# Kernel tuning notes

Measured on AMD Instinct MI355X. Metric: run time of the kernel, lower is better.

The kernel has to match this reference:

```python
import jax, jax.numpy as jnp
import numpy as np

B, H = 1024, 256
HP = H // 2  # hyperparams_dim
W_SCALE = 0.08  # kaiming-uniform-like magnitude to keep tanh unsaturated


def setup_inputs() -> dict:
    key = jax.random.key(0)
    ks = jax.random.split(key, 8)
    return {
        "h_0": jax.random.normal(ks[0], (B, 1, H), dtype=jnp.float32),
        "h_t": jax.random.normal(ks[1], (B, 1, H), dtype=jnp.float32),
        "msg": jax.random.normal(ks[2], (B, 1, H), dtype=jnp.float32),
        "c": jax.random.uniform(ks[3], (1,), dtype=jnp.float32),
        "fc1_w": jax.random.normal(ks[4], (HP, H), dtype=jnp.float32) * W_SCALE,
        "fc2_w": jax.random.normal(ks[5], (HP, HP), dtype=jnp.float32) * W_SCALE,
        "fc3_w": jax.random.normal(ks[6], (HP, HP), dtype=jnp.float32) * W_SCALE,
        "fc4_w": jax.random.normal(ks[7], (2 * H * H, HP), dtype=jnp.float32) * W_SCALE,
    }


def reference(h_0, h_t, msg, c, fc1_w, fc2_w, fc3_w, fc4_w):
    # torch code clamps self.c into [0, 1] before use
    cc = jnp.clip(c, 0.0, 1.0)
    h = cc * h_0 + (1.0 - cc) * h_t                     # [B, 1, H]
    x = jnp.tanh(jnp.einsum('bsh,ph->bsp', h, fc1_w))    # [B, 1, HP]
    x = jnp.tanh(jnp.einsum('bsp,qp->bsq', x, fc2_w))    # [B, 1, HP]
    x = jnp.tanh(jnp.einsum('bsq,rq->bsr', x, fc3_w))    # [B, 1, HP]
    f4 = jnp.einsum('bsr,wr->bsw', x, fc4_w)             # [B, 1, 2*H*H]
    g1 = f4[..., : H * H].reshape(-1, H, H)              # [B, H, H]
    g2 = f4[..., H * H :].reshape(-1, H, H)              # [B, H, H]
    # F.linear(msg[i], g) == msg[i] @ g.T, batched over B
    g1_out = jnp.tanh(jnp.einsum('bsh,bkh->bsk', msg, g1))  # [B, 1, H]
    out = jnp.einsum('bsk,bok->bso', g1_out, g2)             # [B, 1, H]
    return out
```

## Files before the change

### kernel.cpp

```cpp
#include <hip/hip_runtime.h>
#include <hip/hip_bf16.h>

#define HDIM 256
#define HPDIM 128

typedef short bf8 __attribute__((ext_vector_type(8)));
typedef float f32x4 __attribute__((ext_vector_type(4)));

__device__ inline unsigned pkbf2(float a, float b) {
  float2 f; f.x = a; f.y = b;
  __hip_bfloat162 h = __float22bfloat162_rn(f);
  unsigned u; __builtin_memcpy(&u, &h, 4); return u;
}
__device__ inline unsigned short bfbits(float v) {
  __hip_bfloat16 h = __float2bfloat16(v);
  unsigned short u; __builtin_memcpy(&u, &h, 2); return u;
}
__device__ inline uint4 pack8u(float4 a, float4 b) {
  uint4 r;
  r.x = pkbf2(a.x, a.y); r.y = pkbf2(a.z, a.w);
  r.z = pkbf2(b.x, b.y); r.w = pkbf2(b.z, b.w);
  return r;
}
__device__ inline float fast_tanh(float x) {
  float t = __expf(2.0f * x);
  return 1.0f - 2.0f * __builtin_amdgcn_rcpf(t + 1.0f);
}
__device__ inline bf8 wfrag(const float* __restrict__ s) {
  float4 a = *(const float4*)s, b = *(const float4*)(s + 4);
  uint4 u = pack8u(a, b);
  bf8 r; __builtin_memcpy(&r, &u, 16); return r;
}

typedef const __attribute__((address_space(1))) unsigned int* gas_ptr;
typedef __attribute__((address_space(3))) unsigned int* las_ptr;
__device__ inline void gld_lds16(const void* g, void* l) {
  __builtin_amdgcn_global_load_lds((gas_ptr)g, (las_ptr)l, 16, 0, 0);
}

__global__ __launch_bounds__(256) void k_prep(
    const float* __restrict__ h0, const float* __restrict__ htv,
    const float* __restrict__ cp,
    const float* __restrict__ w1, const float* __restrict__ w2,
    const float* __restrict__ w3, const float* __restrict__ msg,
    short* __restrict__ x3f, float* __restrict__ msgTT) {
  const int t = threadIdx.x;
  const int bx = blockIdx.x;

  if (bx >= 64) {
    const int b0 = (bx - 64) * 64;
    #pragma unroll
    for (int it = 0; it < 16; ++it) {
      int u = it * 256 + t;
      int bl = u & 63, g = u >> 6;
      float4 v = *(const float4*)(msg + (size_t)(b0 + bl) * HDIM + g * 4);
      *(float4*)(msgTT + (size_t)g * 4096 + (b0 + bl) * 4) = v;
    }
    return;
  }

  __shared__ char hbuf[8192];
  __shared__ char xa[4096];
  __shared__ char xb[4096];
  const int wave = t >> 6, lane = t & 63;
  const int r16 = lane & 15, quad = lane >> 4;
  const int b0 = bx * 16;
  const float cc = fminf(fmaxf(cp[0], 0.f), 1.f);

  #pragma unroll
  for (int it = 0; it < 2; ++it) {
    int flat = it * 2048 + t * 8;
    int row = flat >> 8, col = flat & 255, kb = col >> 3;
    int gi = (b0 + row) * HDIM + col;
    float4 a = *(const float4*)(h0 + gi);
    float4 b = *(const float4*)(htv + gi);
    float4 va, vb;
    va.x = cc*a.x + (1.f-cc)*b.x; va.y = cc*a.y + (1.f-cc)*b.y;
    va.z = cc*a.z + (1.f-cc)*b.z; va.w = cc*a.w + (1.f-cc)*b.w;
    a = *(const float4*)(h0 + gi + 4); b = *(const float4*)(htv + gi + 4);
    vb.x = cc*a.x + (1.f-cc)*b.x; vb.y = cc*a.y + (1.f-cc)*b.y;
    vb.z = cc*a.z + (1.f-cc)*b.z; vb.w = cc*a.w + (1.f-cc)*b.w;
    *(uint4*)(hbuf + row*512 + ((kb ^ (row & 7)) << 4)) = pack8u(va, vb);
  }
  __syncthreads();

  {
    f32x4 acc[2] = {};
    #pragma unroll
    for (int ks = 0; ks < 8; ++ks) {
      bf8 af = *(bf8*)(hbuf + r16*512 + (((ks*4 + quad) ^ (r16 & 7)) << 4));
      #pragma unroll
      for (int nt = 0; nt < 2; ++nt) {
        bf8 bw_ = wfrag(w1 + ((wave*2 + nt)*16 + r16) * 256 + ks*32 + quad*8);
        acc[nt] = __builtin_amdgcn_mfma_f32_16x16x32_bf16(af, bw_, acc[nt], 0, 0, 0);
      }
    }
    #pragma unroll
    for (int nt = 0; nt < 2; ++nt)
      #pragma unroll
      for (int i = 0; i < 4; ++i) {
        int row = quad*4 + i, col = wave*32 + nt*16 + r16;
        *(unsigned short*)(xa + row*256 + (((col >> 3) ^ (row & 7)) << 4) + ((col & 7) << 1))
            = bfbits(fast_tanh(acc[nt][i]));
      }
  }
  __syncthreads();
  {
    f32x4 acc[2] = {};
    #pragma unroll
    for (int ks = 0; ks < 4; ++ks) {
      bf8 af = *(bf8*)(xa + r16*256 + (((ks*4 + quad) ^ (r16 & 7)) << 4));
      #pragma unroll
      for (int nt = 0; nt < 2; ++nt) {
        bf8 bw_ = wfrag(w2 + ((wave*2 + nt)*16 + r16) * 128 + ks*32 + quad*8);
        acc[nt] = __builtin_amdgcn_mfma_f32_16x16x32_bf16(af, bw_, acc[nt], 0, 0, 0);
      }
    }
    #pragma unroll
    for (int nt = 0; nt < 2; ++nt)
      #pragma unroll
      for (int i = 0; i < 4; ++i) {
        int row = quad*4 + i, col = wave*32 + nt*16 + r16;
        *(unsigned short*)(xb + row*256 + (((col >> 3) ^ (row & 7)) << 4) + ((col & 7) << 1))
            = bfbits(fast_tanh(acc[nt][i]));
      }
  }
  __syncthreads();
  {
    f32x4 acc[2] = {};
    #pragma unroll
    for (int ks = 0; ks < 4; ++ks) {
      bf8 af = *(bf8*)(xb + r16*256 + (((ks*4 + quad) ^ (r16 & 7)) << 4));
      #pragma unroll
      for (int nt = 0; nt < 2; ++nt) {
        bf8 bw_ = wfrag(w3 + ((wave*2 + nt)*16 + r16) * 128 + ks*32 + quad*8);
        acc[nt] = __builtin_amdgcn_mfma_f32_16x16x32_bf16(af, bw_, acc[nt], 0, 0, 0);
      }
    }
    #pragma unroll
    for (int nt = 0; nt < 2; ++nt)
      #pragma unroll
      for (int i = 0; i < 4; ++i) {
        int row = quad*4 + i, col = wave*32 + nt*16 + r16;
        *(unsigned short*)(xa + row*256 + (((col >> 3) ^ (row & 7)) << 4) + ((col & 7) << 1))
            = bfbits(fast_tanh(acc[nt][i]));
      }
  }
  __syncthreads();
  {
    int ks = t >> 6, l = t & 63, q2 = l >> 4, rr = l & 15;
    uint4 d = *(uint4*)(xa + rr*256 + (((ks*4 + q2) ^ (rr & 7)) << 4));
    *(uint4*)(x3f + (size_t)((bx*4 + ks)*64 + l)*8) = d;
  }
}

template<int PHASE>
__global__ __launch_bounds__(512, 2) void k_hyper(
    const short* __restrict__ x3f, const float* __restrict__ wTT,
    const float* __restrict__ fc4, float* __restrict__ outp) {
  __shared__ char lds[65536 + 16384];
  char* slab = lds;
  char* ring = lds + 65536;
  const int bxs = blockIdx.x;
  const int h = bxs >> 8;
  const int p = bxs & 255;
  const int kcol = ((p & 7) << 5) | (p >> 3);
  const int t = threadIdx.x, wave = t >> 6, lane = t & 63;
  const int r16 = lane & 15, quad = lane >> 4;
  const int bw = h * 512 + wave * 64;

  const float* src = fc4 + ((size_t)(PHASE ? 65536 : 0) + (size_t)kcol * 256) * HPDIM;

  gld_lds16(src + t * 4, ring + t * 16);

  bf8 xf[4][4];
  #pragma unroll
  for (int nt = 0; nt < 4; ++nt)
    #pragma unroll
    for (int ks = 0; ks < 4; ++ks)
      xf[nt][ks] = *(const bf8*)(x3f +
          (size_t)(((h*32 + wave*4 + nt)*4 + ks)*64 + lane)*8);
  #pragma unroll
  for (int nt = 0; nt < 4; ++nt)
    #pragma unroll
    for (int ks = 0; ks < 4; ++ks)
      asm volatile("" : "+v"(xf[nt][ks]));

  asm volatile("s_waitcnt vmcnt(0) lgkmcnt(0)" ::: "memory");
  __builtin_amdgcn_sched_barrier(0);
  {
    f32x4 v = *(const f32x4*)(ring + t * 16);
    int row = t >> 5, kb = (t & 31) >> 1;
    uint2 o; o.x = pkbf2(v[0], v[1]); o.y = pkbf2(v[2], v[3]);
    *(uint2*)(slab + row * 256 + ((kb ^ (row & 7)) << 4) + (t & 1) * 8) = o;
  }
  gld_lds16(src + 2048 + t * 4, ring + 8192 + t * 16);
  asm volatile("s_waitcnt lgkmcnt(0)" ::: "memory");
  __builtin_amdgcn_sched_barrier(0);
  __builtin_amdgcn_s_barrier();

  float gacc[4] = {0.f, 0.f, 0.f, 0.f};
  const float* wbase = wTT + (size_t)quad * 4096 + (bw + r16) * 4;

  #pragma unroll 1
  for (int c = 0; c < 16; ++c) {
    {
      float4 wv[4];
      #pragma unroll
      for (int nt = 0; nt < 4; ++nt)
        wv[nt] = *(const float4*)(wbase + (size_t)c*16384 + nt*64);
      const int row = c*16 + r16;
      bf8 af[4];
      #pragma unroll
      for (int ks = 0; ks < 4; ++ks)
        af[ks] = *(bf8*)(slab + row*256 + (((ks*4 + quad) ^ (r16 & 7)) << 4));
      #pragma unroll
      for (int nt = 0; nt < 4; ++nt) {
        f32x4 acc = {};
        #pragma unroll
        for (int ks = 0; ks < 4; ++ks)
          acc = __builtin_amdgcn_mfma_f32_16x16x32_bf16(af[ks], xf[nt][ks], acc, 0, 0, 0);
        gacc[nt] += acc[0]*wv[nt].x + acc[1]*wv[nt].y + acc[2]*wv[nt].z + acc[3]*wv[nt].w;
      }
    }
    if (c < 15) {
      asm volatile("s_waitcnt vmcnt(0)" ::: "memory");
      __builtin_amdgcn_sched_barrier(0);
      if (c + 2 < 16)
        gld_lds16(src + (c + 2) * 2048 + t * 4, ring + ((c + 2) & 1) * 8192 + t * 16);
      {
        f32x4 v = *(const f32x4*)(ring + ((c + 1) & 1) * 8192 + t * 16);
        int row = (c + 1) * 16 + (t >> 5), kb = (t & 31) >> 1;
        uint2 o; o.x = pkbf2(v[0], v[1]); o.y = pkbf2(v[2], v[3]);
        *(uint2*)(slab + row * 256 + ((kb ^ ((t >> 5) & 7)) << 4) + (t & 1) * 8) = o;
      }
      asm volatile("s_waitcnt lgkmcnt(0)" ::: "memory");
      __builtin_amdgcn_sched_barrier(0);
      __builtin_amdgcn_s_barrier();
    }
  }

  #pragma unroll
  for (int nt = 0; nt < 4; ++nt) {
    float v = gacc[nt];
    v += __shfl_xor(v, 16);
    v += __shfl_xor(v, 32);
    if (quad == 0) {
      int b = bw + nt*16 + r16;
      if (PHASE == 0) outp[(size_t)(kcol >> 2)*4096 + b*4 + (kcol & 3)] = fast_tanh(v);
      else            outp[b*HDIM + kcol] = v;
    }
  }
}

extern "C" void kernel_launch(void* const* d_in, const int* in_sizes, int n_in,
                              void* d_out, int out_size, void* d_ws, size_t ws_size,
                              hipStream_t stream) {
  const float* h0  = (const float*)d_in[0];
  const float* htt = (const float*)d_in[1];
  const float* msg = (const float*)d_in[2];
  const float* c   = (const float*)d_in[3];
  const float* w1  = (const float*)d_in[4];
  const float* w2  = (const float*)d_in[5];
  const float* w3  = (const float*)d_in[6];
  const float* w4  = (const float*)d_in[7];
  float* out = (float*)d_out;

  short* x3f  = (short*)d_ws;
  float* g1TT = (float*)((char*)d_ws + 262144);
  float* msgTT= (float*)((char*)d_ws + 262144 + 1048576);

  k_prep<<<dim3(80), dim3(256), 0, stream>>>(h0, htt, c, w1, w2, w3, msg,
                                             x3f, msgTT);
  k_hyper<0><<<dim3(512), dim3(512), 0, stream>>>(x3f, msgTT, w4, g1TT);
  k_hyper<1><<<dim3(512), dim3(512), 0, stream>>>(x3f, g1TT, w4, out);
}
```

Baseline: 159.4 us.

## Process both batch halves per block, reusing converted fc4 slab; interleave MFMA chains

Each block now covers all 1024 batch rows instead of one half, so every fc4 column slab is loaded from HBM and converted to bf16 only once instead of twice. The grid shrinks from 512 to 256 blocks. A second pass reuses the resident LDS slab with freshly loaded x fragments for the second batch half. The MFMA loop is also rewritten into four independent accumulator chains wrapped in raised wave priority, which should improve MFMA issue overlap. The cost is fewer blocks (one per CU on 256 CUs) and a serialized second pass per block.

```diff
diff --git a/kernel.cpp b/kernel.cpp
--- a/kernel.cpp
+++ b/kernel.cpp
@@ -161,13 +161,10 @@
   __shared__ char lds[65536 + 16384];
   char* slab = lds;
   char* ring = lds + 65536;
-  const int bxs = blockIdx.x;
-  const int h = bxs >> 8;
-  const int p = bxs & 255;
+  const int p = blockIdx.x;
   const int kcol = ((p & 7) << 5) | (p >> 3);
   const int t = threadIdx.x, wave = t >> 6, lane = t & 63;
   const int r16 = lane & 15, quad = lane >> 4;
-  const int bw = h * 512 + wave * 64;
 
   const float* src = fc4 + ((size_t)(PHASE ? 65536 : 0) + (size_t)kcol * 256) * HPDIM;
 
@@ -179,7 +176,7 @@
     #pragma unroll
     for (int ks = 0; ks < 4; ++ks)
       xf[nt][ks] = *(const bf8*)(x3f +
-          (size_t)(((h*32 + wave*4 + nt)*4 + ks)*64 + lane)*8);
+          (size_t)(((wave*4 + nt)*4 + ks)*64 + lane)*8);
   #pragma unroll
   for (int nt = 0; nt < 4; ++nt)
     #pragma unroll
@@ -200,7 +197,7 @@
   __builtin_amdgcn_s_barrier();
 
   float gacc[4] = {0.f, 0.f, 0.f, 0.f};
-  const float* wbase = wTT + (size_t)quad * 4096 + (bw + r16) * 4;
+  const float* wbase = wTT + (size_t)quad * 4096 + (wave * 64 + r16) * 4;
 
   #pragma unroll 1
   for (int c = 0; c < 16; ++c) {
@@ -214,14 +211,20 @@
       #pragma unroll
       for (int ks = 0; ks < 4; ++ks)
         af[ks] = *(bf8*)(slab + row*256 + (((ks*4 + quad) ^ (r16 & 7)) << 4));
-      #pragma unroll
-      for (int nt = 0; nt < 4; ++nt) {
-        f32x4 acc = {};
-        #pragma unroll
-        for (int ks = 0; ks < 4; ++ks)
-          acc = __builtin_amdgcn_mfma_f32_16x16x32_bf16(af[ks], xf[nt][ks], acc, 0, 0, 0);
-        gacc[nt] += acc[0]*wv[nt].x + acc[1]*wv[nt].y + acc[2]*wv[nt].z + acc[3]*wv[nt].w;
-      }
+      __builtin_amdgcn_s_setprio(1);
+      f32x4 acc0 = {}, acc1 = {}, acc2 = {}, acc3 = {};
+      #pragma unroll
+      for (int ks = 0; ks < 4; ++ks) {
+        acc0 = __builtin_amdgcn_mfma_f32_16x16x32_bf16(af[ks], xf[0][ks], acc0, 0, 0, 0);
+        acc1 = __builtin_amdgcn_mfma_f32_16x16x32_bf16(af[ks], xf[1][ks], acc1, 0, 0, 0);
+        acc2 = __builtin_amdgcn_mfma_f32_16x16x32_bf16(af[ks], xf[2][ks], acc2, 0, 0, 0);
+        acc3 = __builtin_amdgcn_mfma_f32_16x16x32_bf16(af[ks], xf[3][ks], acc3, 0, 0, 0);
+      }
+      __builtin_amdgcn_s_setprio(0);
+      gacc[0] += acc0[0]*wv[0].x + acc0[1]*wv[0].y + acc0[2]*wv[0].z + acc0[3]*wv[0].w;
+      gacc[1] += acc1[0]*wv[1].x + acc1[1]*wv[1].y + acc1[2]*wv[1].z + acc1[3]*wv[1].w;
+      gacc[2] += acc2[0]*wv[2].x + acc2[1]*wv[2].y + acc2[2]*wv[2].z + acc2[3]*wv[2].w;
+      gacc[3] += acc3[0]*wv[3].x + acc3[1]*wv[3].y + acc3[2]*wv[3].z + acc3[3]*wv[3].w;
     }
     if (c < 15) {
       asm volatile("s_waitcnt vmcnt(0)" ::: "memory");
@@ -239,14 +242,65 @@
       __builtin_amdgcn_s_barrier();
     }
   }
-
   #pragma unroll
   for (int nt = 0; nt < 4; ++nt) {
     float v = gacc[nt];
     v += __shfl_xor(v, 16);
     v += __shfl_xor(v, 32);
     if (quad == 0) {
-      int b = bw + nt*16 + r16;
+      int b = wave*64 + nt*16 + r16;
+      if (PHASE == 0) outp[(size_t)(kcol >> 2)*4096 + b*4 + (kcol & 3)] = fast_tanh(v);
+      else            outp[b*HDIM + kcol] = v;
+    }
+  }
+
+  #pragma unroll
+  for (int nt = 0; nt < 4; ++nt)
+    #pragma unroll
+    for (int ks = 0; ks < 4; ++ks)
+      xf[nt][ks] = *(const bf8*)(x3f +
+          (size_t)(((32 + wave*4 + nt)*4 + ks)*64 + lane)*8);
+  #pragma unroll
+  for (int nt = 0; nt < 4; ++nt)
+    #pragma unroll
+    for (int ks = 0; ks < 4; ++ks)
+      asm volatile("" : "+v"(xf[nt][ks]));
+  gacc[0] = gacc[1] = gacc[2] = gacc[3] = 0.f;
+  const float* wbase2 = wTT + (size_t)quad * 4096 + (512 + wave * 64 + r16) * 4;
+
+  #pragma unroll 1
+  for (int hg = 0; hg < 16; ++hg) {
+    float4 wv[4];
+    #pragma unroll
+    for (int nt = 0; nt < 4; ++nt)
+      wv[nt] = *(const float4*)(wbase2 + (size_t)hg*16384 + nt*64);
+    const int row = hg*16 + r16;
+    bf8 af[4];
+    #pragma unroll
+    for (int ks = 0; ks < 4; ++ks)
+      af[ks] = *(bf8*)(slab + row*256 + (((ks*4 + quad) ^ (r16 & 7)) << 4));
+    __builtin_amdgcn_s_setprio(1);
+    f32x4 acc0 = {}, acc1 = {}, acc2 = {}, acc3 = {};
+    #pragma unroll
+    for (int ks = 0; ks < 4; ++ks) {
+      acc0 = __builtin_amdgcn_mfma_f32_16x16x32_bf16(af[ks], xf[0][ks], acc0, 0, 0, 0);
+      acc1 = __builtin_amdgcn_mfma_f32_16x16x32_bf16(af[ks], xf[1][ks], acc1, 0, 0, 0);
+      acc2 = __builtin_amdgcn_mfma_f32_16x16x32_bf16(af[ks], xf[2][ks], acc2, 0, 0, 0);
+      acc3 = __builtin_amdgcn_mfma_f32_16x16x32_bf16(af[ks], xf[3][ks], acc3, 0, 0, 0);
+    }
+    __builtin_amdgcn_s_setprio(0);
+    gacc[0] += acc0[0]*wv[0].x + acc0[1]*wv[0].y + acc0[2]*wv[0].z + acc0[3]*wv[0].w;
+    gacc[1] += acc1[0]*wv[1].x + acc1[1]*wv[1].y + acc1[2]*wv[1].z + acc1[3]*wv[1].w;
+    gacc[2] += acc2[0]*wv[2].x + acc2[1]*wv[2].y + acc2[2]*wv[2].z + acc2[3]*wv[2].w;
+    gacc[3] += acc3[0]*wv[3].x + acc3[1]*wv[3].y + acc3[2]*wv[3].z + acc3[3]*wv[3].w;
+  }
+  #pragma unroll
+  for (int nt = 0; nt < 4; ++nt) {
+    float v = gacc[nt];
+    v += __shfl_xor(v, 16);
+    v += __shfl_xor(v, 32);
+    if (quad == 0) {
+      int b = 512 + wave*64 + nt*16 + r16;
       if (PHASE == 0) outp[(size_t)(kcol >> 2)*4096 + b*4 + (kcol & 3)] = fast_tanh(v);
       else            outp[b*HDIM + kcol] = v;
     }
@@ -272,6 +326,6 @@
 
   k_prep<<<dim3(80), dim3(256), 0, stream>>>(h0, htt, c, w1, w2, w3, msg,
                                              x3f, msgTT);
-  k_hyper<0><<<dim3(512), dim3(512), 0, stream>>>(x3f, msgTT, w4, g1TT);
-  k_hyper<1><<<dim3(512), dim3(512), 0, stream>>>(x3f, g1TT, w4, out);
-}
+  k_hyper<0><<<dim3(256), dim3(512), 0, stream>>>(x3f, msgTT, w4, g1TT);
+  k_hyper<1><<<dim3(256), dim3(512), 0, stream>>>(x3f, g1TT, w4, out);
+}
```

Result: slower. 170.0 us (+6.6%).
